# Performance work log

Hardware: AMD Instinct MI355X
Metric: run time of the kernel (lower is better)

## Reference

```python
import jax, jax.numpy as jnp
import numpy as np

N = 100000      # nodes
E = 3200000     # edges (avg degree 32)
IN_DIM = 256
OUT_DIM = 256


def setup_inputs() -> dict:
    key = jax.random.key(0)
    k1, k2, k3, k4, k5, k6 = jax.random.split(key, 6)
    row = jax.random.randint(k1, (E,), 0, N, dtype=jnp.int32)
    col = jax.random.randint(k2, (E,), 0, N, dtype=jnp.int32)
    vals = jax.random.uniform(k3, (E,), dtype=jnp.float32)
    x = jax.random.normal(k4, (N, IN_DIM), dtype=jnp.float32)
    W = jax.random.normal(k5, (IN_DIM, OUT_DIM), dtype=jnp.float32) * (IN_DIM ** -0.5)
    b = jax.random.normal(k6, (OUT_DIM,), dtype=jnp.float32) * 0.01
    return {"row": row, "col": col, "vals": vals, "x": x, "W": W, "b": b}


def reference(row, col, vals, x, W, b):
    # H = A_hat @ x  (sparse COO matmul via gather + segment-sum scatter)
    gathered = vals[:, None] * x[col]              # [E, in_dim]
    agg = jax.ops.segment_sum(gathered, row, num_segments=N)  # [N, in_dim]
    # Dense linear: agg @ W + b
    return agg @ W + b                             # [N, out_dim]
```

## Files before the change

### kernel.cpp

```cpp
#include <hip/hip_runtime.h>

#define IN_DIM 256
#define OUT_DIM 256
#define NBITS 8
#define CHUNK 8192
#define CAP 13056
#define VAL_SCALE 32767.0f
#define INV_VAL_SCALE (1.0f / 32767.0f)

typedef __attribute__((ext_vector_type(8))) short bf16x8;
typedef __attribute__((ext_vector_type(4))) float f32x4;

static __device__ __forceinline__ unsigned short f2bf(float f) {
    unsigned int u = __float_as_uint(f);
    u = (u + 0x7FFFu + ((u >> 16) & 1u)) >> 16;
    return (unsigned short)u;
}

__global__ __launch_bounds__(256) void prep_kernel(const float* __restrict__ W,
                                                   unsigned short* __restrict__ Wb,
                                                   int* __restrict__ cursor, int nb) {
    int blk = blockIdx.x;
    int t = threadIdx.x;
    if (blk < 256) {
        int idx = blk * 256 + t;
        int k = idx >> 8, c = idx & 255;
        Wb[(c >> 4) * 4096 + (k >> 3) * 128 + (c & 15) * 8 + (k & 7)] = f2bf(W[idx]);
    } else {
        for (int i = t; i < nb; i += 256) cursor[i] = i * CAP;
    }
}

__global__ __launch_bounds__(512) void bucket_scatter(const int* __restrict__ row,
                                                      const int* __restrict__ col,
                                                      const float* __restrict__ vals,
                                                      int* __restrict__ cursor,
                                                      unsigned int* __restrict__ edge_p,
                                                      unsigned char* __restrict__ rowloc,
                                                      int E, int nb) {
    __shared__ int hist[512];
    __shared__ int gbase[512];
    __shared__ int cur[512];
    const int t = threadIdx.x;
    const int base_e = blockIdx.x * CHUNK;

    int bk_s[CHUNK / 512];
    unsigned int pay_s[CHUNK / 512];
    unsigned char rl_s[CHUNK / 512];

    for (int i = t; i < nb; i += 512) { hist[i] = 0; cur[i] = 0; }
    __syncthreads();
#pragma unroll
    for (int i = 0; i < CHUNK / 512; ++i) {
        int e = base_e + i * 512 + t;
        if (e < E) {
            int r = row[e];
            int bk = r >> NBITS;
            unsigned int vq = (unsigned int)(vals[e] * VAL_SCALE + 0.5f);
            bk_s[i] = bk;
            pay_s[i] = ((unsigned int)col[e] << 15) | vq;
            rl_s[i] = (unsigned char)(r & 255);
            atomicAdd(&hist[bk], 1);
        } else {
            bk_s[i] = -1;
        }
    }
    __syncthreads();
    for (int i = t; i < nb; i += 512) {
        int c = hist[i];
        if (c > 0) gbase[i] = atomicAdd(&cursor[i], c);
    }
    __syncthreads();
#pragma unroll
    for (int i = 0; i < CHUNK / 512; ++i) {
        int bk = bk_s[i];
        if (bk >= 0) {
            int loc = atomicAdd(&cur[bk], 1);
            int dest = gbase[bk] + loc;
            edge_p[dest] = pay_s[i];
            rowloc[dest] = rl_s[i];
        }
    }
}

__global__ __launch_bounds__(512) void permute_gemm_fused(
        const int* __restrict__ cursor, unsigned int* __restrict__ edge_p,
        const unsigned char* __restrict__ rowloc, int2* __restrict__ row_se,
        int N, int nb,
        const float* __restrict__ x, const unsigned short* __restrict__ Wb,
        unsigned short* __restrict__ y, int M) {
    __shared__ unsigned int ep[CAP];
    __shared__ unsigned char rl[CAP];
    __shared__ int cnt[256];
    __shared__ int cur[256];
    __shared__ int fin[256];
    __shared__ int wsum[4];

    const int t = threadIdx.x;
    if (blockIdx.x < (unsigned)nb) {
        const int b = blockIdx.x;
        const int gb = b * CAP;
        int m = cursor[b] - gb;
        if (m > CAP) m = CAP;
        if (t < 256) cnt[t] = 0;
        __syncthreads();
        for (int i = t; i < m; i += 512) {
            ep[i] = edge_p[gb + i];
            unsigned char r = rowloc[gb + i];
            rl[i] = r;
            atomicAdd(&cnt[r], 1);
        }
        __syncthreads();
        int pcv = 0, incl = 0;
        const int lane = t & 63;
        const int w = t >> 6;
        if (t < 256) {
            pcv = (cnt[t] + 3) & ~3;
            incl = pcv;
#pragma unroll
            for (int off = 1; off < 64; off <<= 1) {
                int u = __shfl_up(incl, off, 64);
                if (lane >= off) incl += u;
            }
            if (lane == 63) wsum[w] = incl;
        }
        __syncthreads();
        if (t < 256) {
            int wp = 0;
            for (int k = 0; k < w; ++k) wp += wsum[k];
            int excl = wp + incl - pcv;
            cur[t] = excl;
            fin[t] = excl + pcv;
            const int baseRow = b << NBITS;
            if (t < N - baseRow)
                row_se[baseRow + t] = make_int2(gb + excl, gb + excl + pcv);
        }
        __syncthreads();
        for (int i = t; i < m; i += 512) {
            int r = rl[i];
            int pos = atomicAdd(&cur[r], 1);
            edge_p[gb + pos] = ep[i];
        }
        __syncthreads();
        if (t < 256) {
            for (int pos = cur[t]; pos < fin[t]; ++pos)
                edge_p[gb + pos] = 0u;
        }
    } else {
        const int gblk = blockIdx.x - nb;
        const int lane = t & 63;
        const int wid = t >> 6;
        const int wr = wid >> 2;
        const int wc = wid & 3;
        const int r0 = gblk * 128 + wr * 64;
        const int c0 = wc * 64;

        f32x4 acc[4][4];
#pragma unroll
        for (int m = 0; m < 4; ++m)
#pragma unroll
            for (int n = 0; n < 4; ++n) acc[m][n] = (f32x4){0.f, 0.f, 0.f, 0.f};

        const int arow_off = lane & 15;
        const int kgrp = lane >> 4;

#pragma unroll
        for (int step = 0; step < 8; ++step) {
            const int k0 = step * 32 + kgrp * 8;
            bf16x8 a[4], bfr[4];
#pragma unroll
            for (int m = 0; m < 4; ++m) {
                int rr = r0 + m * 16 + arow_off;
                rr = min(rr, M - 1);
                const float* xr = x + (size_t)rr * IN_DIM + k0;
                float4 f0 = *reinterpret_cast<const float4*>(xr);
                float4 f1 = *reinterpret_cast<const float4*>(xr + 4);
                a[m][0] = (short)f2bf(f0.x); a[m][1] = (short)f2bf(f0.y);
                a[m][2] = (short)f2bf(f0.z); a[m][3] = (short)f2bf(f0.w);
                a[m][4] = (short)f2bf(f1.x); a[m][5] = (short)f2bf(f1.y);
                a[m][6] = (short)f2bf(f1.z); a[m][7] = (short)f2bf(f1.w);
            }
#pragma unroll
            for (int n = 0; n < 4; ++n) {
                int nbk = wc * 4 + n;
                bfr[n] = *reinterpret_cast<const bf16x8*>(
                    Wb + (size_t)nbk * 4096 + (step * 4 + kgrp) * 128 + arow_off * 8);
            }
#pragma unroll
            for (int m = 0; m < 4; ++m)
#pragma unroll
                for (int n = 0; n < 4; ++n)
                    acc[m][n] = __builtin_amdgcn_mfma_f32_16x16x32_bf16(a[m], bfr[n], acc[m][n], 0, 0, 0);
        }

#pragma unroll
        for (int m = 0; m < 4; ++m) {
            int rbase = r0 + m * 16 + kgrp * 4;
#pragma unroll
            for (int i = 0; i < 4; ++i) {
                int rr = rbase + i;
                if (rr < M) {
                    unsigned short* yr = y + (size_t)rr * OUT_DIM + c0 + arow_off;
#pragma unroll
                    for (int n = 0; n < 4; ++n) yr[n * 16] = f2bf(acc[m][n][i]);
                }
            }
        }
    }
}

__global__ __launch_bounds__(1024) void aggregate_rows_bf16(const int2* __restrict__ row_se,
                                                            const unsigned int* __restrict__ edge_p,
                                                            const unsigned short* __restrict__ y,
                                                            const float* __restrict__ b,
                                                            float* __restrict__ out, int N) {
    const int lane = threadIdx.x & 63;
    const int w = threadIdx.x >> 6;
    const int r = blockIdx.x * 16 + w;
    if (r >= N) return;

    const int2 se = row_se[r];
    const int start = se.x;
    const int end = se.y;
    const int half = lane >> 5;
    const int d0 = (lane & 31) * 8;

    float acc[8];
#pragma unroll
    for (int i = 0; i < 8; ++i) acc[i] = 0.f;

    int j = start;
    for (; j + 8 <= end; j += 8) {
        uint4 mp = *reinterpret_cast<const uint4*>(edge_p + j + half * 4);
        float v0 = (float)(mp.x & 0x7fffu) * INV_VAL_SCALE;
        float v1 = (float)(mp.y & 0x7fffu) * INV_VAL_SCALE;
        float v2 = (float)(mp.z & 0x7fffu) * INV_VAL_SCALE;
        float v3 = (float)(mp.w & 0x7fffu) * INV_VAL_SCALE;
        uint4 u0 = *reinterpret_cast<const uint4*>(y + ((size_t)(mp.x >> 15)) * OUT_DIM + d0);
        uint4 u1 = *reinterpret_cast<const uint4*>(y + ((size_t)(mp.y >> 15)) * OUT_DIM + d0);
        uint4 u2 = *reinterpret_cast<const uint4*>(y + ((size_t)(mp.z >> 15)) * OUT_DIM + d0);
        uint4 u3 = *reinterpret_cast<const uint4*>(y + ((size_t)(mp.w >> 15)) * OUT_DIM + d0);
        acc[0] += v0 * __uint_as_float(u0.x << 16);
        acc[1] += v0 * __uint_as_float(u0.x & 0xffff0000u);
        acc[2] += v0 * __uint_as_float(u0.y << 16);
        acc[3] += v0 * __uint_as_float(u0.y & 0xffff0000u);
        acc[4] += v0 * __uint_as_float(u0.z << 16);
        acc[5] += v0 * __uint_as_float(u0.z & 0xffff0000u);
        acc[6] += v0 * __uint_as_float(u0.w << 16);
        acc[7] += v0 * __uint_as_float(u0.w & 0xffff0000u);
        acc[0] += v1 * __uint_as_float(u1.x << 16);
        acc[1] += v1 * __uint_as_float(u1.x & 0xffff0000u);
        acc[2] += v1 * __uint_as_float(u1.y << 16);
        acc[3] += v1 * __uint_as_float(u1.y & 0xffff0000u);
        acc[4] += v1 * __uint_as_float(u1.z << 16);
        acc[5] += v1 * __uint_as_float(u1.z & 0xffff0000u);
        acc[6] += v1 * __uint_as_float(u1.w << 16);
        acc[7] += v1 * __uint_as_float(u1.w & 0xffff0000u);
        acc[0] += v2 * __uint_as_float(u2.x << 16);
        acc[1] += v2 * __uint_as_float(u2.x & 0xffff0000u);
        acc[2] += v2 * __uint_as_float(u2.y << 16);
        acc[3] += v2 * __uint_as_float(u2.y & 0xffff0000u);
        acc[4] += v2 * __uint_as_float(u2.z << 16);
        acc[5] += v2 * __uint_as_float(u2.z & 0xffff0000u);
        acc[6] += v2 * __uint_as_float(u2.w << 16);
        acc[7] += v2 * __uint_as_float(u2.w & 0xffff0000u);
        acc[0] += v3 * __uint_as_float(u3.x << 16);
        acc[1] += v3 * __uint_as_float(u3.x & 0xffff0000u);
        acc[2] += v3 * __uint_as_float(u3.y << 16);
        acc[3] += v3 * __uint_as_float(u3.y & 0xffff0000u);
        acc[4] += v3 * __uint_as_float(u3.z << 16);
        acc[5] += v3 * __uint_as_float(u3.z & 0xffff0000u);
        acc[6] += v3 * __uint_as_float(u3.w << 16);
        acc[7] += v3 * __uint_as_float(u3.w & 0xffff0000u);
    }
    if (j < end) {
        uint2 mp = *reinterpret_cast<const uint2*>(edge_p + j + half * 2);
        float v0 = (float)(mp.x & 0x7fffu) * INV_VAL_SCALE;
        float v1 = (float)(mp.y & 0x7fffu) * INV_VAL_SCALE;
        uint4 u0 = *reinterpret_cast<const uint4*>(y + ((size_t)(mp.x >> 15)) * OUT_DIM + d0);
        uint4 u1 = *reinterpret_cast<const uint4*>(y + ((size_t)(mp.y >> 15)) * OUT_DIM + d0);
        acc[0] += v0 * __uint_as_float(u0.x << 16);
        acc[1] += v0 * __uint_as_float(u0.x & 0xffff0000u);
        acc[2] += v0 * __uint_as_float(u0.y << 16);
        acc[3] += v0 * __uint_as_float(u0.y & 0xffff0000u);
        acc[4] += v0 * __uint_as_float(u0.z << 16);
        acc[5] += v0 * __uint_as_float(u0.z & 0xffff0000u);
        acc[6] += v0 * __uint_as_float(u0.w << 16);
        acc[7] += v0 * __uint_as_float(u0.w & 0xffff0000u);
        acc[0] += v1 * __uint_as_float(u1.x << 16);
        acc[1] += v1 * __uint_as_float(u1.x & 0xffff0000u);
        acc[2] += v1 * __uint_as_float(u1.y << 16);
        acc[3] += v1 * __uint_as_float(u1.y & 0xffff0000u);
        acc[4] += v1 * __uint_as_float(u1.z << 16);
        acc[5] += v1 * __uint_as_float(u1.z & 0xffff0000u);
        acc[6] += v1 * __uint_as_float(u1.w << 16);
        acc[7] += v1 * __uint_as_float(u1.w & 0xffff0000u);
    }

#pragma unroll
    for (int i = 0; i < 8; ++i) acc[i] += __shfl_xor(acc[i], 32, 64);

    if (half == 0) {
        float4 b0 = *reinterpret_cast<const float4*>(b + d0);
        float4 b1 = *reinterpret_cast<const float4*>(b + d0 + 4);
        float4 o0 = make_float4(acc[0] + b0.x, acc[1] + b0.y, acc[2] + b0.z, acc[3] + b0.w);
        float4 o1 = make_float4(acc[4] + b1.x, acc[5] + b1.y, acc[6] + b1.z, acc[7] + b1.w);
        float* op = out + (size_t)r * OUT_DIM + d0;
        *reinterpret_cast<float4*>(op) = o0;
        *reinterpret_cast<float4*>(op + 4) = o1;
    }
}

extern "C" void kernel_launch(void* const* d_in, const int* in_sizes, int n_in,
                              void* d_out, int out_size, void* d_ws, size_t ws_size,
                              hipStream_t stream) {
    const int*   row  = (const int*)d_in[0];
    const int*   col  = (const int*)d_in[1];
    const float* vals = (const float*)d_in[2];
    const float* x    = (const float*)d_in[3];
    const float* W    = (const float*)d_in[4];
    const float* b    = (const float*)d_in[5];
    const int E = in_sizes[0];
    const int N = in_sizes[3] / IN_DIM;
    const int nb = (N + 255) >> NBITS;

    float* out = (float*)d_out;

    char* ws = (char*)d_ws;
    size_t off = 0;
    unsigned short* y = (unsigned short*)(ws + off);  off += (size_t)N * OUT_DIM * 2;
    off = (off + 255) & ~(size_t)255;
    unsigned short* Wb = (unsigned short*)(ws + off); off += (size_t)IN_DIM * OUT_DIM * 2;
    off = (off + 255) & ~(size_t)255;
    unsigned int* edge_p = (unsigned int*)(ws + off); off += (size_t)nb * CAP * 4;
    unsigned char* rowloc = (unsigned char*)(ws + off); off += (size_t)nb * CAP;
    off = (off + 255) & ~(size_t)255;
    int* cursor = (int*)(ws + off);                   off += (size_t)nb * 4;
    off = (off + 255) & ~(size_t)255;
    int2* row_se = (int2*)(ws + off);                 off += (size_t)N * 8;

    const int GB = (N + 127) / 128;
    const int SB = (E + CHUNK - 1) / CHUNK;

    prep_kernel<<<257, 256, 0, stream>>>(W, Wb, cursor, nb);

    bucket_scatter<<<SB, 512, 0, stream>>>(row, col, vals, cursor,
                                           edge_p, rowloc, E, nb);

    permute_gemm_fused<<<nb + GB, 512, 0, stream>>>(cursor, edge_p, rowloc, row_se,
                                                    N, nb, x, Wb, y, N);

    aggregate_rows_bf16<<<(N + 15) / 16, 1024, 0, stream>>>(row_se, edge_p, y, b, out, N);
}
```

Before: 387.5 us.

## Split dense GEMM tiles across scatter and permute kernels to overlap work

Moves the dense x@W tile computation into a shared device helper and splits the tiles between two launches. About three fifths of the GEMM tiles now run alongside the bucket scatter, and the rest stay with the permute kernel. The aim is to fill idle compute units while the scatter kernel is bound by atomics and memory, shortening the critical path. The trade-off is extra register pressure in the scatter kernel, which may lower its occupancy, and a fixed split ratio.

```diff
diff --git a/kernel.cpp b/kernel.cpp
--- a/kernel.cpp
+++ b/kernel.cpp
@@ -15,6 +15,70 @@
     unsigned int u = __float_as_uint(f);
     u = (u + 0x7FFFu + ((u >> 16) & 1u)) >> 16;
     return (unsigned short)u;
+}
+
+static __device__ __forceinline__ void gemm_tile(int gblk, const float* __restrict__ x,
+                                                 const unsigned short* __restrict__ Wb,
+                                                 unsigned short* __restrict__ y, int M,
+                                                 int t) {
+    const int lane = t & 63;
+    const int wid = t >> 6;
+    const int wr = wid >> 2;
+    const int wc = wid & 3;
+    const int r0 = gblk * 128 + wr * 64;
+    const int c0 = wc * 64;
+
+    f32x4 acc[4][4];
+#pragma unroll
+    for (int m = 0; m < 4; ++m)
+#pragma unroll
+        for (int n = 0; n < 4; ++n) acc[m][n] = (f32x4){0.f, 0.f, 0.f, 0.f};
+
+    const int arow_off = lane & 15;
+    const int kgrp = lane >> 4;
+
+#pragma unroll
+    for (int step = 0; step < 8; ++step) {
+        const int k0 = step * 32 + kgrp * 8;
+        bf16x8 a[4], bfr[4];
+#pragma unroll
+        for (int m = 0; m < 4; ++m) {
+            int rr = r0 + m * 16 + arow_off;
+            rr = min(rr, M - 1);
+            const float* xr = x + (size_t)rr * IN_DIM + k0;
+            float4 f0 = *reinterpret_cast<const float4*>(xr);
+            float4 f1 = *reinterpret_cast<const float4*>(xr + 4);
+            a[m][0] = (short)f2bf(f0.x); a[m][1] = (short)f2bf(f0.y);
+            a[m][2] = (short)f2bf(f0.z); a[m][3] = (short)f2bf(f0.w);
+            a[m][4] = (short)f2bf(f1.x); a[m][5] = (short)f2bf(f1.y);
+            a[m][6] = (short)f2bf(f1.z); a[m][7] = (short)f2bf(f1.w);
+        }
+#pragma unroll
+        for (int n = 0; n < 4; ++n) {
+            int nbk = wc * 4 + n;
+            bfr[n] = *reinterpret_cast<const bf16x8*>(
+                Wb + (size_t)nbk * 4096 + (step * 4 + kgrp) * 128 + arow_off * 8);
+        }
+#pragma unroll
+        for (int m = 0; m < 4; ++m)
+#pragma unroll
+            for (int n = 0; n < 4; ++n)
+                acc[m][n] = __builtin_amdgcn_mfma_f32_16x16x32_bf16(a[m], bfr[n], acc[m][n], 0, 0, 0);
+    }
+
+#pragma unroll
+    for (int m = 0; m < 4; ++m) {
+        int rbase = r0 + m * 16 + kgrp * 4;
+#pragma unroll
+        for (int i = 0; i < 4; ++i) {
+            int rr = rbase + i;
+            if (rr < M) {
+                unsigned short* yr = y + (size_t)rr * OUT_DIM + c0 + arow_off;
+#pragma unroll
+                for (int n = 0; n < 4; ++n) yr[n * 16] = f2bf(acc[m][n][i]);
+            }
+        }
+    }
 }
 
 __global__ __launch_bounds__(256) void prep_kernel(const float* __restrict__ W,
@@ -31,62 +95,69 @@
     }
 }
 
-__global__ __launch_bounds__(512) void bucket_scatter(const int* __restrict__ row,
-                                                      const int* __restrict__ col,
-                                                      const float* __restrict__ vals,
-                                                      int* __restrict__ cursor,
-                                                      unsigned int* __restrict__ edge_p,
-                                                      unsigned char* __restrict__ rowloc,
-                                                      int E, int nb) {
+__global__ __launch_bounds__(512) void scatter_gemm1(const int* __restrict__ row,
+                                                     const int* __restrict__ col,
+                                                     const float* __restrict__ vals,
+                                                     int* __restrict__ cursor,
+                                                     unsigned int* __restrict__ edge_p,
+                                                     unsigned char* __restrict__ rowloc,
+                                                     int E, int nb, int SB,
+                                                     const float* __restrict__ x,
+                                                     const unsigned short* __restrict__ Wb,
+                                                     unsigned short* __restrict__ y, int M) {
     __shared__ int hist[512];
     __shared__ int gbase[512];
     __shared__ int cur[512];
     const int t = threadIdx.x;
-    const int base_e = blockIdx.x * CHUNK;
-
-    int bk_s[CHUNK / 512];
-    unsigned int pay_s[CHUNK / 512];
-    unsigned char rl_s[CHUNK / 512];
-
-    for (int i = t; i < nb; i += 512) { hist[i] = 0; cur[i] = 0; }
-    __syncthreads();
-#pragma unroll
-    for (int i = 0; i < CHUNK / 512; ++i) {
-        int e = base_e + i * 512 + t;
-        if (e < E) {
-            int r = row[e];
-            int bk = r >> NBITS;
-            unsigned int vq = (unsigned int)(vals[e] * VAL_SCALE + 0.5f);
-            bk_s[i] = bk;
-            pay_s[i] = ((unsigned int)col[e] << 15) | vq;
-            rl_s[i] = (unsigned char)(r & 255);
-            atomicAdd(&hist[bk], 1);
-        } else {
-            bk_s[i] = -1;
-        }
-    }
-    __syncthreads();
-    for (int i = t; i < nb; i += 512) {
-        int c = hist[i];
-        if (c > 0) gbase[i] = atomicAdd(&cursor[i], c);
-    }
-    __syncthreads();
-#pragma unroll
-    for (int i = 0; i < CHUNK / 512; ++i) {
-        int bk = bk_s[i];
-        if (bk >= 0) {
-            int loc = atomicAdd(&cur[bk], 1);
-            int dest = gbase[bk] + loc;
-            edge_p[dest] = pay_s[i];
-            rowloc[dest] = rl_s[i];
-        }
-    }
-}
-
-__global__ __launch_bounds__(512) void permute_gemm_fused(
+
+    if (blockIdx.x < (unsigned)SB) {
+        const int base_e = blockIdx.x * CHUNK;
+        int bk_s[CHUNK / 512];
+        unsigned int pay_s[CHUNK / 512];
+        unsigned char rl_s[CHUNK / 512];
+
+        for (int i = t; i < nb; i += 512) { hist[i] = 0; cur[i] = 0; }
+        __syncthreads();
+#pragma unroll
+        for (int i = 0; i < CHUNK / 512; ++i) {
+            int e = base_e + i * 512 + t;
+            if (e < E) {
+                int r = row[e];
+                int bk = r >> NBITS;
+                unsigned int vq = (unsigned int)(vals[e] * VAL_SCALE + 0.5f);
+                bk_s[i] = bk;
+                pay_s[i] = ((unsigned int)col[e] << 15) | vq;
+                rl_s[i] = (unsigned char)(r & 255);
+                atomicAdd(&hist[bk], 1);
+            } else {
+                bk_s[i] = -1;
+            }
+        }
+        __syncthreads();
+        for (int i = t; i < nb; i += 512) {
+            int c = hist[i];
+            if (c > 0) gbase[i] = atomicAdd(&cursor[i], c);
+        }
+        __syncthreads();
+#pragma unroll
+        for (int i = 0; i < CHUNK / 512; ++i) {
+            int bk = bk_s[i];
+            if (bk >= 0) {
+                int loc = atomicAdd(&cur[bk], 1);
+                int dest = gbase[bk] + loc;
+                edge_p[dest] = pay_s[i];
+                rowloc[dest] = rl_s[i];
+            }
+        }
+    } else {
+        gemm_tile(blockIdx.x - SB, x, Wb, y, M, t);
+    }
+}
+
+__global__ __launch_bounds__(512) void permute_gemm2(
         const int* __restrict__ cursor, unsigned int* __restrict__ edge_p,
         const unsigned char* __restrict__ rowloc, int2* __restrict__ row_se,
-        int N, int nb,
+        int N, int nb, int G2,
         const float* __restrict__ x, const unsigned short* __restrict__ Wb,
         unsigned short* __restrict__ y, int M) {
     __shared__ unsigned int ep[CAP];
@@ -147,65 +218,7 @@
                 edge_p[gb + pos] = 0u;
         }
     } else {
-        const int gblk = blockIdx.x - nb;
-        const int lane = t & 63;
-        const int wid = t >> 6;
-        const int wr = wid >> 2;
-        const int wc = wid & 3;
-        const int r0 = gblk * 128 + wr * 64;
-        const int c0 = wc * 64;
-
-        f32x4 acc[4][4];
-#pragma unroll
-        for (int m = 0; m < 4; ++m)
-#pragma unroll
-            for (int n = 0; n < 4; ++n) acc[m][n] = (f32x4){0.f, 0.f, 0.f, 0.f};
-
-        const int arow_off = lane & 15;
-        const int kgrp = lane >> 4;
-
-#pragma unroll
-        for (int step = 0; step < 8; ++step) {
-            const int k0 = step * 32 + kgrp * 8;
-            bf16x8 a[4], bfr[4];
-#pragma unroll
-            for (int m = 0; m < 4; ++m) {
-                int rr = r0 + m * 16 + arow_off;
-                rr = min(rr, M - 1);
-                const float* xr = x + (size_t)rr * IN_DIM + k0;
-                float4 f0 = *reinterpret_cast<const float4*>(xr);
-                float4 f1 = *reinterpret_cast<const float4*>(xr + 4);
-                a[m][0] = (short)f2bf(f0.x); a[m][1] = (short)f2bf(f0.y);
-                a[m][2] = (short)f2bf(f0.z); a[m][3] = (short)f2bf(f0.w);
-                a[m][4] = (short)f2bf(f1.x); a[m][5] = (short)f2bf(f1.y);
-                a[m][6] = (short)f2bf(f1.z); a[m][7] = (short)f2bf(f1.w);
-            }
-#pragma unroll
-            for (int n = 0; n < 4; ++n) {
-                int nbk = wc * 4 + n;
-                bfr[n] = *reinterpret_cast<const bf16x8*>(
-                    Wb + (size_t)nbk * 4096 + (step * 4 + kgrp) * 128 + arow_off * 8);
-            }
-#pragma unroll
-            for (int m = 0; m < 4; ++m)
-#pragma unroll
-                for (int n = 0; n < 4; ++n)
-                    acc[m][n] = __builtin_amdgcn_mfma_f32_16x16x32_bf16(a[m], bfr[n], acc[m][n], 0, 0, 0);
-        }
-
-#pragma unroll
-        for (int m = 0; m < 4; ++m) {
-            int rbase = r0 + m * 16 + kgrp * 4;
-#pragma unroll
-            for (int i = 0; i < 4; ++i) {
-                int rr = rbase + i;
-                if (rr < M) {
-                    unsigned short* yr = y + (size_t)rr * OUT_DIM + c0 + arow_off;
-#pragma unroll
-                    for (int n = 0; n < 4; ++n) yr[n * 16] = f2bf(acc[m][n][i]);
-                }
-            }
-        }
+        gemm_tile(G2 + (blockIdx.x - nb), x, Wb, y, M, t);
     }
 }
 
@@ -341,14 +354,16 @@
 
     const int GB = (N + 127) / 128;
     const int SB = (E + CHUNK - 1) / CHUNK;
+    const int G2 = (GB * 3) / 5;
 
     prep_kernel<<<257, 256, 0, stream>>>(W, Wb, cursor, nb);
 
-    bucket_scatter<<<SB, 512, 0, stream>>>(row, col, vals, cursor,
-                                           edge_p, rowloc, E, nb);
-
-    permute_gemm_fused<<<nb + GB, 512, 0, stream>>>(cursor, edge_p, rowloc, row_se,
-                                                    N, nb, x, Wb, y, N);
+    scatter_gemm1<<<SB + G2, 512, 0, stream>>>(row, col, vals, cursor,
+                                               edge_p, rowloc, E, nb, SB,
+                                               x, Wb, y, N);
+
+    permute_gemm2<<<nb + (GB - G2), 512, 0, stream>>>(cursor, edge_p, rowloc, row_se,
+                                                      N, nb, G2, x, Wb, y, N);
 
     aggregate_rows_bf16<<<(N + 15) / 16, 1024, 0, stream>>>(row_se, edge_p, y, b, out, N);
 }
```

Result: faster. 379.6 us (-2.0%).
